# Kernel tuning notes

Measured on AMD Instinct MI355X. Metric: run time of the kernel, lower is better.

Reference implementation:

```python
import jax, jax.numpy as jnp
import numpy as np

L, B, N, D, H, DH, MLP = 4, 4, 2048, 512, 8, 64, 2048
EPS = 1e-5


def layer_norm(x, w, b):
    mu = jnp.mean(x, axis=-1, keepdims=True)
    var = jnp.mean(jnp.square(x - mu), axis=-1, keepdims=True)
    return (x - mu) * jax.lax.rsqrt(var + EPS) * w + b


def setup_inputs() -> dict:
    key = jax.random.key(0)
    ks = jax.random.split(key, 8)
    x = jax.random.normal(ks[0], (B, N, D), dtype=jnp.float32)
    # mask == 1.0 means blocked: triu(ones) - eye -> strict upper triangle
    mask = jnp.triu(jnp.ones((N, N), dtype=jnp.float32)) - jnp.eye(N, dtype=jnp.float32)
    s = 0.02
    return {
        "x": x,
        "mask": mask,
        "ln1_w": jnp.ones((L, D), jnp.float32),
        "ln1_b": jnp.zeros((L, D), jnp.float32),
        "w_qkv": jax.random.normal(ks[1], (L, D, 3 * H * DH), jnp.float32) * s,
        "w_out": jax.random.normal(ks[2], (L, H * DH, D), jnp.float32) * s,
        "b_out": jnp.zeros((L, D), jnp.float32),
        "ln2_w": jnp.ones((L, D), jnp.float32),
        "ln2_b": jnp.zeros((L, D), jnp.float32),
        "w1": jax.random.normal(ks[3], (L, D, MLP), jnp.float32) * s,
        "b1": jnp.zeros((L, MLP), jnp.float32),
        "w2": jax.random.normal(ks[4], (L, MLP, D), jnp.float32) * s,
        "b2": jnp.zeros((L, D), jnp.float32),
    }


def reference(x, mask, ln1_w, ln1_b, w_qkv, w_out, b_out, ln2_w, ln2_b, w1, b1, w2, b2):
    scale = DH ** (-0.5)
    blocked = (mask == 1.0)  # [N, N]
    for l in range(L):
        # --- masked self-attention (pre-norm) ---
        h = layer_norm(x, ln1_w[l], ln1_b[l])
        qkv = h @ w_qkv[l]                               # [B, N, 3*H*DH]
        q, k, v = jnp.split(qkv, 3, axis=-1)
        q = q.reshape(B, N, H, DH).transpose(0, 2, 1, 3)  # bhnd
        k = k.reshape(B, N, H, DH).transpose(0, 2, 1, 3)
        v = v.reshape(B, N, H, DH).transpose(0, 2, 1, 3)
        scores = jnp.einsum('bhnd,bhmd->bhnm', q, k) * scale
        scores = jnp.where(blocked, -jnp.inf, scores)
        att = jax.nn.softmax(scores, axis=-1)
        o = jnp.einsum('bhnm,bhmd->bhnd', att, v)
        o = o.transpose(0, 2, 1, 3).reshape(B, N, H * DH)
        x = x + (o @ w_out[l] + b_out[l])
        # --- GELU MLP (pre-norm) ---
        h2 = layer_norm(x, ln2_w[l], ln2_b[l])
        ff = jax.nn.gelu(h2 @ w1[l] + b1[l], approximate=False) @ w2[l] + b2[l]
        x = x + ff
    return x
```

## Files before the change

### kernel.cpp

```cpp
#include <hip/hip_runtime.h>
#include <math.h>

#define L 4
#define BATCH 4
#define N 2048
#define D 512
#define H 8
#define DH 64
#define MLPD 2048
#define M_ROWS (BATCH * N)
#define VTP 2064

using v8s = __attribute__((ext_vector_type(8))) short;
using v4f = __attribute__((ext_vector_type(4))) float;

__device__ inline short f2bf(float f) {
  union { float f; unsigned u; } v; v.f = f;
  unsigned r = v.u + 0x7FFFu + ((v.u >> 16) & 1u);
  return (short)(r >> 16);
}
__device__ inline short f2bf_t(float f) {
  union { float f; unsigned u; } v; v.f = f;
  return (short)(v.u >> 16);
}

#define MFMA(a, b, c) __builtin_amdgcn_mfma_f32_16x16x32_bf16(a, b, c, 0, 0, 0)

__device__ __forceinline__ void gload_lds16(const void* g, void* l) {
  __builtin_amdgcn_global_load_lds((const __attribute__((address_space(1))) void*)g,
                                   (__attribute__((address_space(3))) void*)l, 16, 0, 0);
}

__global__ void copyf4_kernel(const float4* __restrict__ in, float4* __restrict__ out, int n) {
  int i = blockIdx.x * blockDim.x + threadIdx.x;
  if (i < n) out[i] = in[i];
}

__launch_bounds__(256)
__global__ void transpose_w_kernel(const float* __restrict__ src, short* __restrict__ dst,
                                   int R, int C) {
  __shared__ float tile[32][33];
  const size_t base = (size_t)blockIdx.z * R * C;
  const int c0 = blockIdx.x * 32, r0 = blockIdx.y * 32;
  const int tx = threadIdx.x & 31, ty = threadIdx.x >> 5;
  #pragma unroll
  for (int i = ty; i < 32; i += 8)
    tile[i][tx] = src[base + (size_t)(r0 + i) * C + c0 + tx];
  __syncthreads();
  #pragma unroll
  for (int i = ty; i < 32; i += 8)
    dst[base + (size_t)(c0 + i) * R + r0 + tx] = f2bf(tile[tx][i]);
}

__launch_bounds__(256)
__global__ void ln_kernel(const float* __restrict__ x, const float* __restrict__ w,
                          const float* __restrict__ b, short* __restrict__ out) {
  const int row = blockIdx.x * 4 + (threadIdx.x >> 6);
  const int lane = threadIdx.x & 63;
  const float* xr = x + (size_t)row * D;
  float4 a0 = *(const float4*)(xr + lane * 8);
  float4 a1 = *(const float4*)(xr + lane * 8 + 4);
  float v[8] = {a0.x, a0.y, a0.z, a0.w, a1.x, a1.y, a1.z, a1.w};
  float s = 0.f;
  #pragma unroll
  for (int j = 0; j < 8; ++j) s += v[j];
  #pragma unroll
  for (int m = 1; m < 64; m <<= 1) s += __shfl_xor(s, m, 64);
  const float mean = s * (1.0f / D);
  float q = 0.f;
  #pragma unroll
  for (int j = 0; j < 8; ++j) { float d = v[j] - mean; q += d * d; }
  #pragma unroll
  for (int m = 1; m < 64; m <<= 1) q += __shfl_xor(q, m, 64);
  const float rstd = rsqrtf(q * (1.0f / D) + 1e-5f);
  float4 w0 = *(const float4*)(w + lane * 8);
  float4 w1 = *(const float4*)(w + lane * 8 + 4);
  float4 b0 = *(const float4*)(b + lane * 8);
  float4 b1 = *(const float4*)(b + lane * 8 + 4);
  float wv[8] = {w0.x, w0.y, w0.z, w0.w, w1.x, w1.y, w1.z, w1.w};
  float bv[8] = {b0.x, b0.y, b0.z, b0.w, b1.x, b1.y, b1.z, b1.w};
  v8s r;
  #pragma unroll
  for (int j = 0; j < 8; ++j) r[j] = f2bf((v[j] - mean) * rstd * wv[j] + bv[j]);
  *(v8s*)(out + (size_t)row * D + lane * 8) = r;
}

template <int MODE, int BN>
__launch_bounds__(256)
__global__ void gemm128_kernel(const short* __restrict__ A, const short* __restrict__ Bt,
                               const float* __restrict__ bias, const float* __restrict__ Xres,
                               void* __restrict__ Out, int M, int Nc, int K) {
  constexpr int MR = (BN == 128) ? 4 : 2;
  __shared__ __align__(16) short As[2][128 * 64];
  __shared__ __align__(16) short Bs[2][BN * 64];
  const int tid = threadIdx.x;
  const int lane = tid & 63;
  const int w = tid >> 6;
  const int wr = (BN == 128) ? (w >> 1) : w;
  const int wc = (BN == 128) ? (w & 1) : 0;
  const int r16 = lane & 15, g = lane >> 4;

  const int nxb = Nc / BN;
  const int nyb = M >> 7;
  const int bid = (int)blockIdx.x;
  const int xcd = bid & 7;
  const int ii = bid >> 3;
  const int byi = xcd * (nyb >> 3) + ii / nxb;
  const int bxi = ii % nxb;
  const int m0 = byi * 128, n0 = bxi * BN;

  const int srow = lane >> 3;
  const int ssw = ((lane & 7) ^ srow) * 8;

  auto STAGE = [&](int buf, int k0) {
    #pragma unroll
    for (int j = 0; j < 4; ++j) {
      const int row = w * 32 + j * 8;
      gload_lds16(A + (size_t)(m0 + row + srow) * K + k0 + ssw,
                  (char*)&As[buf][0] + row * 128);
    }
    #pragma unroll
    for (int j = 0; j < BN / 32; ++j) {
      const int row = w * (BN / 4) + j * 8;
      gload_lds16(Bt + (size_t)(n0 + row + srow) * K + k0 + ssw,
                  (char*)&Bs[buf][0] + row * 128);
    }
  };

  v4f acc[MR][4] = {};

  STAGE(0, 0);
  __syncthreads();
  int cur = 0;
  for (int k0 = 0; k0 < K; k0 += 64) {
    if (k0 + 64 < K) STAGE(cur ^ 1, k0 + 64);
    v8s af[MR][2], bf[4][2];
    #pragma unroll
    for (int m = 0; m < MR; ++m) {
      const int row = wr * (MR * 16) + m * 16 + r16;
      #pragma unroll
      for (int kh = 0; kh < 2; ++kh)
        af[m][kh] = *(const v8s*)((const char*)&As[cur][0] + row * 128 +
                                  (((kh * 4 + g) ^ (row & 7)) * 16));
    }
    #pragma unroll
    for (int n = 0; n < 4; ++n) {
      const int row = wc * 64 + n * 16 + r16;
      #pragma unroll
      for (int kh = 0; kh < 2; ++kh)
        bf[n][kh] = *(const v8s*)((const char*)&Bs[cur][0] + row * 128 +
                                  (((kh * 4 + g) ^ (row & 7)) * 16));
    }
    #pragma unroll
    for (int kh = 0; kh < 2; ++kh)
      #pragma unroll
      for (int m = 0; m < MR; ++m)
        #pragma unroll
        for (int n = 0; n < 4; ++n)
          acc[m][n] = MFMA(af[m][kh], bf[n][kh], acc[m][n]);
    __syncthreads();
    cur ^= 1;
  }

  #pragma unroll
  for (int m = 0; m < MR; ++m) {
    const int row = m0 + wr * (MR * 16) + m * 16 + g * 4;
    #pragma unroll
    for (int n = 0; n < 4; ++n) {
      const int col = n0 + wc * 64 + n * 16 + r16;
      const float bv = bias ? bias[col] : 0.0f;
      #pragma unroll
      for (int r = 0; r < 4; ++r) {
        const size_t idx = (size_t)(row + r) * Nc + col;
        float val = acc[m][n][r] + bv;
        if constexpr (MODE == 0) {
          ((short*)Out)[idx] = f2bf(val);
        } else if constexpr (MODE == 1) {
          const float z = val * 0.70710678118f;
          const float az = fabsf(z);
          const float t = 1.0f / (1.0f + 0.3275911f * az);
          const float p =
              0.254829592f +
              t * (-0.284496736f + t * (1.421413741f + t * (-1.453152027f + t * 1.061405429f)));
          float er = 1.0f - p * t * __expf(-az * az);
          er = (z < 0.0f) ? -er : er;
          val = 0.5f * val * (1.0f + er);
          ((short*)Out)[idx] = f2bf(val);
        } else {
          ((float*)Out)[idx] = val + Xres[idx];
        }
      }
    }
  }
}

__launch_bounds__(256)
__global__ void kv_prep_kernel(const short* __restrict__ qkv, short* __restrict__ Vt) {
  __shared__ __align__(16) short tile[64][88];
  const int b = blockIdx.z, h = blockIdx.y, n0 = blockIdx.x * 64;
  const int tid = threadIdx.x;
  const int bh = b * H + h;
  const int row2 = tid >> 3, d0 = (tid & 7) * 8;
  #pragma unroll
  for (int i = 0; i < 2; ++i) {
    const int n = i * 32 + row2;
    const short* src = qkv + ((size_t)(b * N + n0 + n)) * 1536 + 1024 + h * 64 + d0;
    *(v8s*)&tile[n][d0] = *(const v8s*)src;
  }
  __syncthreads();
  const int dh = tid & 63, nc = (tid >> 6) * 16;
  #pragma unroll
  for (int j = 0; j < 2; ++j) {
    v8s ov;
    #pragma unroll
    for (int e = 0; e < 8; ++e) ov[e] = tile[nc + j * 8 + e][dh];
    *(v8s*)(Vt + ((size_t)(bh * 64 + dh)) * VTP + n0 + nc + j * 8) = ov;
  }
}

__launch_bounds__(256)
__global__ void attn_kernel(const short* __restrict__ qkv, const short* __restrict__ Vt,
                            short* __restrict__ o) {
  __shared__ __align__(16) short Ks[2][64 * 64];
  __shared__ __align__(16) short Vs[2][64 * 64];
  __shared__ __align__(16) short Pw[4][16 * 72];
  const int lin = (int)blockIdx.x;
  const int bh = ((lin >> 3) & 3) * 8 + (lin & 7);
  const int xl2 = 31 - (lin >> 5);
  const int b = bh >> 3, h = bh & 7;
  const int q0 = xl2 * 64;
  const int tid = threadIdx.x, lane = tid & 63, w = tid >> 6;
  const int r16 = lane & 15, g = lane >> 4;
  const int qw = q0 + w * 16;

  v8s qf0, qf1;
  {
    const size_t qbase = ((size_t)(b * N + qw + r16)) * 1536 + h * 64;
    qf0 = *(const v8s*)(qkv + qbase + g * 8);
    qf1 = *(const v8s*)(qkv + qbase + 32 + g * 8);
  }

  const short* vtb = Vt + (size_t)bh * 64 * VTP;
  short* pw = &Pw[w][0];

  const int srow = lane >> 3;
  const int ssw = ((lane & 7) ^ srow) * 8;

  int fo[4][2];
  #pragma unroll
  for (int a = 0; a < 4; ++a)
    #pragma unroll
    for (int c = 0; c < 2; ++c)
      fo[a][c] = (a * 16 + r16) * 128 + (((c * 4 + g) ^ (r16 & 7)) * 16);

  v4f oacc[4] = {};
  float lrun[4] = {};
  const int tdiag = xl2;

  auto STAGE = [&](int buf, int t) {
    const int k0 = t * 64;
    #pragma unroll
    for (int j = 0; j < 2; ++j) {
      const int row = w * 16 + j * 8 + srow;
      gload_lds16(qkv + ((size_t)(b * N + k0 + row)) * 1536 + 512 + h * 64 + ssw,
                  (char*)&Ks[buf][0] + (w * 16 + j * 8) * 128);
      gload_lds16(vtb + (size_t)row * VTP + k0 + ssw,
                  (char*)&Vs[buf][0] + (w * 16 + j * 8) * 128);
    }
  };

  STAGE(0, 0);
  __syncthreads();
  int cur = 0;
  for (int t = 0; t <= tdiag; ++t) {
    if (t < tdiag) STAGE(cur ^ 1, t + 1);
    const int k0 = t * 64;
    const char* kb = (const char*)&Ks[cur][0];
    const char* vb = (const char*)&Vs[cur][0];
    v8s kf[4][2], vf[4][2];
    #pragma unroll
    for (int a = 0; a < 4; ++a)
      #pragma unroll
      for (int c = 0; c < 2; ++c) {
        kf[a][c] = *(const v8s*)(kb + fo[a][c]);
        vf[a][c] = *(const v8s*)(vb + fo[a][c]);
      }

    __builtin_amdgcn_s_setprio(1);
    v4f s[4];
    #pragma unroll
    for (int kt = 0; kt < 4; ++kt) {
      v4f ss = {};
      ss = MFMA(qf0, kf[kt][0], ss);
      ss = MFMA(qf1, kf[kt][1], ss);
      s[kt] = ss;
    }
    __builtin_amdgcn_s_setprio(0);

    const bool needmask = (t == tdiag);
    #pragma unroll
    for (int r = 0; r < 4; ++r) {
      const int qrow = qw + g * 4 + r;
      float e[4];
      #pragma unroll
      for (int kt = 0; kt < 4; ++kt) {
        float v = s[kt][r] * 0.125f;
        if (needmask && (k0 + kt * 16 + r16 > qrow)) v = -3e38f;
        e[kt] = __expf(v);
      }
      lrun[r] += (e[0] + e[1]) + (e[2] + e[3]);
      #pragma unroll
      for (int kt = 0; kt < 4; ++kt)
        pw[(g * 4 + r) * 72 + kt * 16 + r16] = f2bf_t(e[kt]);
    }

    __builtin_amdgcn_s_setprio(1);
    #pragma unroll
    for (int s2 = 0; s2 < 2; ++s2) {
      v8s pa = *(const v8s*)&pw[r16 * 72 + s2 * 32 + g * 8];
      #pragma unroll
      for (int dt = 0; dt < 4; ++dt)
        oacc[dt] = MFMA(pa, vf[dt][s2], oacc[dt]);
    }
    __builtin_amdgcn_s_setprio(0);

    __syncthreads();
    cur ^= 1;
  }

  #pragma unroll
  for (int r = 0; r < 4; ++r) {
    #pragma unroll
    for (int mm = 1; mm < 16; mm <<= 1) lrun[r] += __shfl_xor(lrun[r], mm, 64);
  }

  #pragma unroll
  for (int dt = 0; dt < 4; ++dt)
    #pragma unroll
    for (int r = 0; r < 4; ++r) {
      const float val = oacc[dt][r] / lrun[r];
      o[((size_t)(b * N + qw + g * 4 + r)) * 512 + h * 64 + dt * 16 + r16] = f2bf(val);
    }
}

extern "C" void kernel_launch(void* const* d_in, const int* in_sizes, int n_in,
                              void* d_out, int out_size, void* d_ws, size_t ws_size,
                              hipStream_t stream) {
  const float* x_in  = (const float*)d_in[0];
  const float* ln1_w = (const float*)d_in[2];
  const float* ln1_b = (const float*)d_in[3];
  const float* w_qkv = (const float*)d_in[4];
  const float* w_out = (const float*)d_in[5];
  const float* b_out = (const float*)d_in[6];
  const float* ln2_w = (const float*)d_in[7];
  const float* ln2_b = (const float*)d_in[8];
  const float* w1    = (const float*)d_in[9];
  const float* b1    = (const float*)d_in[10];
  const float* w2    = (const float*)d_in[11];
  const float* b2    = (const float*)d_in[12];

  char* ws = (char*)d_ws;
  size_t off = 0;
  auto alloc = [&](size_t bytes) { char* p = ws + off; off += (bytes + 255) & ~(size_t)255; return p; };
  short* wqkvT = (short*)alloc((size_t)L * 1536 * 512 * 2);
  short* woutT = (short*)alloc((size_t)L * 512 * 512 * 2);
  short* w1T   = (short*)alloc((size_t)L * 512 * 2048 * 2);
  short* w2T   = (short*)alloc((size_t)L * 2048 * 512 * 2);
  short* hln   = (short*)alloc((size_t)M_ROWS * 512 * 2);
  short* big   = (short*)alloc((size_t)M_ROWS * 2048 * 2);
  short* oatt  = (short*)alloc((size_t)M_ROWS * 512 * 2);
  short* Vtg   = (short*)alloc((size_t)BATCH * H * 64 * VTP * 2);
  short* qkv = big;
  short* ff  = big;

  float* x = (float*)d_out;

  copyf4_kernel<<<4096, 256, 0, stream>>>((const float4*)x_in, (float4*)x, M_ROWS * D / 4);

  transpose_w_kernel<<<dim3(1536 / 32, 512 / 32, L), 256, 0, stream>>>(w_qkv, wqkvT, 512, 1536);
  transpose_w_kernel<<<dim3(512 / 32, 512 / 32, L), 256, 0, stream>>>(w_out, woutT, 512, 512);
  transpose_w_kernel<<<dim3(2048 / 32, 512 / 32, L), 256, 0, stream>>>(w1, w1T, 512, 2048);
  transpose_w_kernel<<<dim3(512 / 32, 2048 / 32, L), 256, 0, stream>>>(w2, w2T, 2048, 512);

  for (int l = 0; l < L; ++l) {
    ln_kernel<<<M_ROWS / 4, 256, 0, stream>>>(x, ln1_w + l * 512, ln1_b + l * 512, hln);
    gemm128_kernel<0, 128><<<dim3((1536 / 128) * (M_ROWS / 128)), 256, 0, stream>>>(
        hln, wqkvT + (size_t)l * 1536 * 512, nullptr, nullptr, qkv, M_ROWS, 1536, 512);
    kv_prep_kernel<<<dim3(N / 64, H, BATCH), 256, 0, stream>>>(qkv, Vtg);
    attn_kernel<<<dim3(1024), 256, 0, stream>>>(qkv, Vtg, oatt);
    gemm128_kernel<2, 64><<<dim3((512 / 64) * (M_ROWS / 128)), 256, 0, stream>>>(
        oatt, woutT + (size_t)l * 512 * 512, b_out + l * 512, x, x, M_ROWS, 512, 512);
    ln_kernel<<<M_ROWS / 4, 256, 0, stream>>>(x, ln2_w + l * 512, ln2_b + l * 512, hln);
    gemm128_kernel<1, 128><<<dim3((2048 / 128) * (M_ROWS / 128)), 256, 0, stream>>>(
        hln, w1T + (size_t)l * 512 * 2048, b1 + l * 2048, nullptr, ff, M_ROWS, 2048, 512);
    gemm128_kernel<2, 64><<<dim3((512 / 64) * (M_ROWS / 128)), 256, 0, stream>>>(
        ff, w2T + (size_t)l * 2048 * 512, b2 + l * 512, x, x, M_ROWS, 512, 2048);
  }
}
```

Before: 689.8 us.

## Compute S transposed so P stays in registers, skipping LDS round-trip in attention

```diff
diff --git a/kernel.cpp b/kernel.cpp
--- a/kernel.cpp
+++ b/kernel.cpp
@@ -19,9 +19,9 @@
   unsigned r = v.u + 0x7FFFu + ((v.u >> 16) & 1u);
   return (short)(r >> 16);
 }
-__device__ inline short f2bf_t(float f) {
-  union { float f; unsigned u; } v; v.f = f;
-  return (short)(v.u >> 16);
+__device__ inline unsigned pack2bf_t(float a, float b) {
+  union { float f; unsigned u; } x, y; x.f = a; y.f = b;
+  return (x.u >> 16) | (y.u & 0xFFFF0000u);
 }
 
 #define MFMA(a, b, c) __builtin_amdgcn_mfma_f32_16x16x32_bf16(a, b, c, 0, 0, 0)
@@ -211,10 +211,14 @@
   const int dh = tid & 63, nc = (tid >> 6) * 16;
   #pragma unroll
   for (int j = 0; j < 2; ++j) {
+    const int oc = nc + j * 8;
+    const int base = (oc >> 5) * 32 + ((oc >> 3) & 3) * 4;
     v8s ov;
     #pragma unroll
-    for (int e = 0; e < 8; ++e) ov[e] = tile[nc + j * 8 + e][dh];
-    *(v8s*)(Vt + ((size_t)(bh * 64 + dh)) * VTP + n0 + nc + j * 8) = ov;
+    for (int e = 0; e < 4; ++e) ov[e] = tile[base + e][dh];
+    #pragma unroll
+    for (int e = 0; e < 4; ++e) ov[4 + e] = tile[base + 16 + e][dh];
+    *(v8s*)(Vt + ((size_t)(bh * 64 + dh)) * VTP + n0 + oc) = ov;
   }
 }
 
@@ -223,7 +227,6 @@
                             short* __restrict__ o) {
   __shared__ __align__(16) short Ks[2][64 * 64];
   __shared__ __align__(16) short Vs[2][64 * 64];
-  __shared__ __align__(16) short Pw[4][16 * 72];
   const int lin = (int)blockIdx.x;
   const int bh = ((lin >> 3) & 3) * 8 + (lin & 7);
   const int xl2 = 31 - (lin >> 5);
@@ -241,20 +244,12 @@
   }
 
   const short* vtb = Vt + (size_t)bh * 64 * VTP;
-  short* pw = &Pw[w][0];
 
   const int srow = lane >> 3;
   const int ssw = ((lane & 7) ^ srow) * 8;
 
-  int fo[4][2];
-  #pragma unroll
-  for (int a = 0; a < 4; ++a)
-    #pragma unroll
-    for (int c = 0; c < 2; ++c)
-      fo[a][c] = (a * 16 + r16) * 128 + (((c * 4 + g) ^ (r16 & 7)) * 16);
-
   v4f oacc[4] = {};
-  float lrun[4] = {};
+  float lsum = 0.f;
   const int tdiag = xl2;
 
   auto STAGE = [&](int buf, int t) {
@@ -277,68 +272,72 @@
     const int k0 = t * 64;
     const char* kb = (const char*)&Ks[cur][0];
     const char* vb = (const char*)&Vs[cur][0];
-    v8s kf[4][2], vf[4][2];
+
+    v8s vf[4][2];
     #pragma unroll
     for (int a = 0; a < 4; ++a)
       #pragma unroll
-      for (int c = 0; c < 2; ++c) {
-        kf[a][c] = *(const v8s*)(kb + fo[a][c]);
-        vf[a][c] = *(const v8s*)(vb + fo[a][c]);
-      }
+      for (int c = 0; c < 2; ++c)
+        vf[a][c] = *(const v8s*)(vb + (a * 16 + r16) * 128 + (((c * 4 + g) ^ (r16 & 7)) * 16));
 
     __builtin_amdgcn_s_setprio(1);
     v4f s[4];
     #pragma unroll
     for (int kt = 0; kt < 4; ++kt) {
+      const int krow = (kt * 16 + r16) * 128;
+      v8s kfa = *(const v8s*)(kb + krow + ((g ^ (r16 & 7)) * 16));
+      v8s kfb = *(const v8s*)(kb + krow + (((4 + g) ^ (r16 & 7)) * 16));
       v4f ss = {};
-      ss = MFMA(qf0, kf[kt][0], ss);
-      ss = MFMA(qf1, kf[kt][1], ss);
+      ss = MFMA(kfa, qf0, ss);
+      ss = MFMA(kfb, qf1, ss);
       s[kt] = ss;
     }
     __builtin_amdgcn_s_setprio(0);
 
     const bool needmask = (t == tdiag);
-    #pragma unroll
-    for (int r = 0; r < 4; ++r) {
-      const int qrow = qw + g * 4 + r;
+    const int qrow = qw + r16;
+    const int kbase = k0 + 4 * g;
+    unsigned pw_[8];
+    #pragma unroll
+    for (int kt = 0; kt < 4; ++kt) {
       float e[4];
       #pragma unroll
-      for (int kt = 0; kt < 4; ++kt) {
+      for (int r = 0; r < 4; ++r) {
         float v = s[kt][r] * 0.125f;
-        if (needmask && (k0 + kt * 16 + r16 > qrow)) v = -3e38f;
-        e[kt] = __expf(v);
+        if (needmask && (kbase + kt * 16 + r > qrow)) v = -3e38f;
+        e[r] = __expf(v);
       }
-      lrun[r] += (e[0] + e[1]) + (e[2] + e[3]);
-      #pragma unroll
-      for (int kt = 0; kt < 4; ++kt)
-        pw[(g * 4 + r) * 72 + kt * 16 + r16] = f2bf_t(e[kt]);
-    }
+      lsum += (e[0] + e[1]) + (e[2] + e[3]);
+      pw_[kt * 2 + 0] = pack2bf_t(e[0], e[1]);
+      pw_[kt * 2 + 1] = pack2bf_t(e[2], e[3]);
+    }
+    union PU { unsigned u[4]; v8s s8; };
+    PU pa0, pa1;
+    pa0.u[0] = pw_[0]; pa0.u[1] = pw_[1]; pa0.u[2] = pw_[2]; pa0.u[3] = pw_[3];
+    pa1.u[0] = pw_[4]; pa1.u[1] = pw_[5]; pa1.u[2] = pw_[6]; pa1.u[3] = pw_[7];
 
     __builtin_amdgcn_s_setprio(1);
     #pragma unroll
-    for (int s2 = 0; s2 < 2; ++s2) {
-      v8s pa = *(const v8s*)&pw[r16 * 72 + s2 * 32 + g * 8];
-      #pragma unroll
-      for (int dt = 0; dt < 4; ++dt)
-        oacc[dt] = MFMA(pa, vf[dt][s2], oacc[dt]);
-    }
+    for (int dt = 0; dt < 4; ++dt) oacc[dt] = MFMA(pa0.s8, vf[dt][0], oacc[dt]);
+    #pragma unroll
+    for (int dt = 0; dt < 4; ++dt) oacc[dt] = MFMA(pa1.s8, vf[dt][1], oacc[dt]);
     __builtin_amdgcn_s_setprio(0);
 
     __syncthreads();
     cur ^= 1;
   }
 
-  #pragma unroll
-  for (int r = 0; r < 4; ++r) {
-    #pragma unroll
-    for (int mm = 1; mm < 16; mm <<= 1) lrun[r] += __shfl_xor(lrun[r], mm, 64);
-  }
+  lsum += __shfl_xor(lsum, 16, 64);
+  lsum += __shfl_xor(lsum, 32, 64);
+  float ldiv[4];
+  #pragma unroll
+  for (int r = 0; r < 4; ++r) ldiv[r] = __shfl(lsum, g * 4 + r, 64);
 
   #pragma unroll
   for (int dt = 0; dt < 4; ++dt)
     #pragma unroll
     for (int r = 0; r < 4; ++r) {
-      const float val = oacc[dt][r] / lrun[r];
+      const float val = oacc[dt][r] / ldiv[r];
       o[((size_t)(b * N + qw + g * 4 + r)) * 512 + h * 64 + dt * 16 + r16] = f2bf(val);
     }
 }
```

Measured after the change: 674.2 us. -2.3%, faster.
